# Performance work log

Measured on AMD Instinct MI355X. Metric: run time of the kernel, lower is better.

Reference implementation:

```python
import jax, jax.numpy as jnp
import numpy as np

COS_EPS = 1e-8   # torch F.cosine_similarity norm clamp
LOG_EPS = 1e-12  # log stabilizer in Sinkhorn
SINK_ITERS = 5
SINK_EPS = 0.5


def _pairwise_cosine(x1, x2):
    # x1, x2: [b, c, hw]; cosine similarity between all channel pairs along hw
    n1 = x1 / jnp.maximum(jnp.linalg.norm(x1, axis=-1, keepdims=True), COS_EPS)
    n2 = x2 / jnp.maximum(jnp.linalg.norm(x2, axis=-1, keepdims=True), COS_EPS)
    return jnp.einsum('bik,bjk->bij', n1, n2)  # [b, c, c]


def _M(C, u, v, eps):
    # C: [b,c,c]; u, v: [b,c,hw]. With b==c==hw this broadcasts to [b,c,hw,hw],
    # exactly mirroring the torch broadcast in the original module.
    return (-C + u[..., None] + v[..., None, :]) / eps


def _sinkhorn(p1, p2, C, iters=SINK_ITERS, eps=SINK_EPS):
    u = jnp.zeros_like(p1)
    v = jnp.zeros_like(p2)
    for _ in range(iters):
        # Gauss-Seidel: v-update uses the freshly updated u (as in the original loop)
        u = eps * (jnp.log(p1 + LOG_EPS)
                   - jax.scipy.special.logsumexp(_M(C, u, v, eps), axis=-1)) + u
        v = eps * (jnp.log(p2 + LOG_EPS)
                   - jax.scipy.special.logsumexp(
                       jnp.swapaxes(_M(C, u, v, eps), -2, -1), axis=-1)) + v
    pi = jnp.exp(_M(C, u, v, eps))
    return jnp.mean(jnp.sum(pi * C, axis=(-2, -1)))


def _emd_single(x1, x2):
    b, c, h, w = x1.shape
    x1 = x1.reshape(b, c, h * w)
    x2 = x2.reshape(b, c, h * w)
    p1 = jax.nn.softmax(x1, axis=-1)  # [b, c, hw]
    p2 = jax.nn.softmax(x2, axis=-1)
    C = 1.0 - _pairwise_cosine(x1, x2)  # [b, c, c]
    Cmin = jnp.min(C, axis=-1, keepdims=True)
    Cmax = jnp.max(C, axis=-1, keepdims=True)
    C = (C - Cmin) / (Cmax - Cmin)
    return _sinkhorn(p1, p2, C)


def setup_inputs() -> dict:
    key = jax.random.key(0)
    k1, k2, k3, k4 = jax.random.split(key, 4)
    B, C, H, W = 64, 64, 8, 8  # requires B == C == H*W (see original broadcast)
    shp = (B, C, H, W)
    return {
        'f1_0': jax.random.normal(k1, shp, dtype=jnp.float32),
        'f1_1': jax.random.normal(k2, shp, dtype=jnp.float32),
        'f2_0': jax.random.normal(k3, shp, dtype=jnp.float32),
        'f2_1': jax.random.normal(k4, shp, dtype=jnp.float32),
    }


def reference(f1_0, f1_1, f2_0, f2_1):
    loss = _emd_single(f1_0, f2_0) + _emd_single(f1_1, f2_1)
    return loss / 2.0
```

## Files before the change

### kernel.cpp

```cpp
#include <hip/hip_runtime.h>
#include <math.h>


#define SINK_ITERS 5
#define LOGEPS 1e-12f
#define COSEPS 1e-8f

typedef __attribute__((ext_vector_type(8))) short bf16x8;
typedef __attribute__((ext_vector_type(4))) float f32x4;

__device__ __forceinline__ float wave_sum(float v) {
    #pragma unroll
    for (int o = 32; o; o >>= 1) v += __shfl_xor(v, o);
    return v;
}
__device__ __forceinline__ float wave_max(float v) {
    #pragma unroll
    for (int o = 32; o; o >>= 1) v = fmaxf(v, __shfl_xor(v, o));
    return v;
}
__device__ __forceinline__ float fast_rcp(float v) {
    return __builtin_amdgcn_rcpf(v);
}
__device__ __forceinline__ unsigned short f2bf(float f) {
    unsigned int u = __float_as_uint(f);
    u = (u + 0x7FFFu + ((u >> 16) & 1u)) >> 16;
    return (unsigned short)u;
}
__device__ __forceinline__ float bf2f(unsigned short h) {
    return __uint_as_float(((unsigned int)h) << 16);
}
__device__ __forceinline__ int frag_idx(int k, int n) {
    return ((k >> 5) << 9) + (((((k & 31) >> 3) << 4) | n) << 3) + (k & 7);
}
__device__ __forceinline__ void split8(const float* f, bf16x8& hi, bf16x8& lo) {
    #pragma unroll
    for (int j = 0; j < 8; j++) {
        unsigned short h = f2bf(f[j]);
        hi[j] = (short)h;
        lo[j] = (short)f2bf(f[j] - bf2f(h));
    }
}
__device__ __forceinline__ void load8(const float* p, float* f) {
    float4 a0 = ((const float4*)p)[0], a1 = ((const float4*)p)[1];
    f[0] = a0.x; f[1] = a0.y; f[2] = a0.z; f[3] = a0.w;
    f[4] = a1.x; f[5] = a1.y; f[6] = a1.z; f[7] = a1.w;
}

__global__ __launch_bounds__(256, 2) void emd_fused(
        const float* __restrict__ f10, const float* __restrict__ f11,
        const float* __restrict__ f20, const float* __restrict__ f21,
        float* __restrict__ out)
{
    __shared__ float Ksh[64][68];
    __shared__ float KTsh[64][68];
    __shared__ float Csh[64][68];
    __shared__ float p1sh[64][17];
    __shared__ float p2sh[64][17];
    __shared__ __align__(16) short aF[1024];
    __shared__ __align__(16) short bF[1024];
    __shared__ float inv1[64], inv2[64];
    __shared__ float wsum[4];

    const int tid = threadIdx.x, w = tid >> 6, lane = tid & 63;
    const int g = blockIdx.x, c = blockIdx.y, p = blockIdx.z;
    const float* x1 = p ? f11 : f10;
    const float* x2 = p ? f21 : f20;

    const int b0 = (g << 4) | (w << 2);
    #pragma unroll
    for (int qq = 0; qq < 4; qq++) {
        const int rowoff = (((b0 + qq) << 6) | c) << 6;
        float xv1 = x1[rowoff + lane];
        float e1 = __expf(xv1 - wave_max(xv1));
        p1sh[lane][(w << 2) + qq] = e1 * fast_rcp(wave_sum(e1)) + LOGEPS;
        float xv2 = x2[rowoff + lane];
        float e2 = __expf(xv2 - wave_max(xv2));
        p2sh[lane][(w << 2) + qq] = e2 * fast_rcp(wave_sum(e2)) + LOGEPS;
    }
    if (tid < 128) {
        bf16x8 one;
        #pragma unroll
        for (int j = 0; j < 8; j++) one[j] = (short)0x3F80;
        *(bf16x8*)&bF[((tid >> 6) << 9) + ((tid & 63) << 3)] = one;
    }

    const int base = c << 12;
    const float4* x1g = (const float4*)(x1 + base);
    const float4* x2g = (const float4*)(x2 + base);
    #pragma unroll
    for (int m = 0; m < 4; m++) {
        int idx = tid + (m << 8);
        int r = idx >> 4, k0 = (idx & 15) << 2;
        *(float4*)&Ksh[r][k0] = x1g[idx];
        *(float4*)&Csh[r][k0] = x2g[idx];
    }
    __syncthreads();

    if (tid < 128) {
        int r = tid & 63;
        const float4* xr = (const float4*)((tid < 64) ? &Ksh[r][0] : &Csh[r][0]);
        float s = 0.f;
        #pragma unroll
        for (int k4 = 0; k4 < 16; k4++) {
            float4 v = xr[k4];
            s += v.x * v.x + v.y * v.y + v.z * v.z + v.w * v.w;
        }
        float inv = 1.0f / fmaxf(sqrtf(s), COSEPS);
        if (tid < 64) inv1[r] = inv; else inv2[r] = inv;
    }
    __syncthreads();

    const int q = lane >> 4, n = lane & 15;
    const int arow = (w << 4) | n;
    bf16x8 Ahi[2], Alo[2];
    #pragma unroll
    for (int ks = 0; ks < 2; ks++) {
        float fa[8];
        load8(&Ksh[arow][(ks << 5) + (q << 3)], fa);
        split8(fa, Ahi[ks], Alo[ks]);
    }
    f32x4 accT[4];
    #pragma unroll
    for (int jt = 0; jt < 4; jt++) {
        bf16x8 Bhi[2], Blo[2];
        #pragma unroll
        for (int ks = 0; ks < 2; ks++) {
            float fb[8];
            load8(&Csh[(jt << 4) | n][(ks << 5) + (q << 3)], fb);
            split8(fb, Bhi[ks], Blo[ks]);
        }
        f32x4 gacc = {0.f, 0.f, 0.f, 0.f};
        gacc = __builtin_amdgcn_mfma_f32_16x16x32_bf16(Ahi[0], Bhi[0], gacc, 0, 0, 0);
        gacc = __builtin_amdgcn_mfma_f32_16x16x32_bf16(Ahi[1], Bhi[1], gacc, 0, 0, 0);
        gacc = __builtin_amdgcn_mfma_f32_16x16x32_bf16(Ahi[0], Blo[0], gacc, 0, 0, 0);
        gacc = __builtin_amdgcn_mfma_f32_16x16x32_bf16(Ahi[1], Blo[1], gacc, 0, 0, 0);
        gacc = __builtin_amdgcn_mfma_f32_16x16x32_bf16(Alo[0], Bhi[0], gacc, 0, 0, 0);
        gacc = __builtin_amdgcn_mfma_f32_16x16x32_bf16(Alo[1], Bhi[1], gacc, 0, 0, 0);
        accT[jt] = gacc;
    }
    __syncthreads();

    #pragma unroll
    for (int reg = 0; reg < 4; reg++) {
        const int i = (w << 4) + (q << 2) + reg;
        const float i1v = inv1[i];
        float cv[4];
        #pragma unroll
        for (int jt = 0; jt < 4; jt++)
            cv[jt] = 1.0f - accT[jt][reg] * i1v * inv2[(jt << 4) | n];
        float mn = fminf(fminf(cv[0], cv[1]), fminf(cv[2], cv[3]));
        float mx = fmaxf(fmaxf(cv[0], cv[1]), fmaxf(cv[2], cv[3]));
        #pragma unroll
        for (int o = 1; o < 16; o <<= 1) {
            mn = fminf(mn, __shfl_xor(mn, o));
            mx = fmaxf(mx, __shfl_xor(mx, o));
        }
        const float irange = fast_rcp(mx - mn);
        #pragma unroll
        for (int jt = 0; jt < 4; jt++) {
            const int j = (jt << 4) | n;
            float cnorm = (cv[jt] - mn) * irange;
            float kv = __expf(-2.0f * cnorm);
            Csh[i][j] = cnorm;
            Ksh[i][j] = kv;
            KTsh[j][i] = kv;
        }
    }
    __syncthreads();

    bf16x8 KhiF[2], KloF[2], KThiF[2], KTloF[2], KChiF[2], KCloF[2];
    #pragma unroll
    for (int ks = 0; ks < 2; ks++) {
        const int k0 = (ks << 5) + (q << 3);
        float fk[8], fkt[8], fkc[8];
        load8(&Ksh[arow][k0], fk);
        load8(&KTsh[arow][k0], fkt);
        load8(&Csh[arow][k0], fkc);
        #pragma unroll
        for (int j = 0; j < 8; j++) fkc[j] *= fk[j];
        split8(fk,  KhiF[ks],  KloF[ks]);
        split8(fkt, KThiF[ks], KTloF[ks]);
        split8(fkc, KChiF[ks], KCloF[ks]);
    }
    float p1r[4], p2r[4], a[4];
    #pragma unroll
    for (int reg = 0; reg < 4; reg++) {
        const int row = (w << 4) + (q << 2) + reg;
        p1r[reg] = p1sh[row][n];
        p2r[reg] = p2sh[row][n];
    }
    __syncthreads();

    #pragma unroll 1
    for (int it = 0; it < SINK_ITERS; it++) {
        bf16x8 bf0 = *(const bf16x8*)&bF[lane << 3];
        bf16x8 bf1 = *(const bf16x8*)&bF[512 + (lane << 3)];
        f32x4 acc = {0.f, 0.f, 0.f, 0.f};
        acc = __builtin_amdgcn_mfma_f32_16x16x32_bf16(KhiF[0], bf0, acc, 0, 0, 0);
        acc = __builtin_amdgcn_mfma_f32_16x16x32_bf16(KhiF[1], bf1, acc, 0, 0, 0);
        acc = __builtin_amdgcn_mfma_f32_16x16x32_bf16(KloF[0], bf0, acc, 0, 0, 0);
        acc = __builtin_amdgcn_mfma_f32_16x16x32_bf16(KloF[1], bf1, acc, 0, 0, 0);
        #pragma unroll
        for (int reg = 0; reg < 4; reg++) {
            a[reg] = p1r[reg] * fast_rcp(acc[reg]);
            aF[frag_idx((w << 4) + (q << 2) + reg, n)] = (short)f2bf(a[reg]);
        }
        __syncthreads();

        bf16x8 af0 = *(const bf16x8*)&aF[lane << 3];
        bf16x8 af1 = *(const bf16x8*)&aF[512 + (lane << 3)];
        f32x4 acc2 = {0.f, 0.f, 0.f, 0.f};
        acc2 = __builtin_amdgcn_mfma_f32_16x16x32_bf16(KThiF[0], af0, acc2, 0, 0, 0);
        acc2 = __builtin_amdgcn_mfma_f32_16x16x32_bf16(KThiF[1], af1, acc2, 0, 0, 0);
        acc2 = __builtin_amdgcn_mfma_f32_16x16x32_bf16(KTloF[0], af0, acc2, 0, 0, 0);
        acc2 = __builtin_amdgcn_mfma_f32_16x16x32_bf16(KTloF[1], af1, acc2, 0, 0, 0);
        #pragma unroll
        for (int reg = 0; reg < 4; reg++) {
            float bnew = p2r[reg] * fast_rcp(acc2[reg]);
            bF[frag_idx((w << 4) + (q << 2) + reg, n)] = (short)f2bf(bnew);
        }
        __syncthreads();
    }

    {
        bf16x8 bf0 = *(const bf16x8*)&bF[lane << 3];
        bf16x8 bf1 = *(const bf16x8*)&bF[512 + (lane << 3)];
        f32x4 acc3 = {0.f, 0.f, 0.f, 0.f};
        acc3 = __builtin_amdgcn_mfma_f32_16x16x32_bf16(KChiF[0], bf0, acc3, 0, 0, 0);
        acc3 = __builtin_amdgcn_mfma_f32_16x16x32_bf16(KChiF[1], bf1, acc3, 0, 0, 0);
        acc3 = __builtin_amdgcn_mfma_f32_16x16x32_bf16(KCloF[0], bf0, acc3, 0, 0, 0);
        acc3 = __builtin_amdgcn_mfma_f32_16x16x32_bf16(KCloF[1], bf1, acc3, 0, 0, 0);
        float part = a[0] * acc3[0] + a[1] * acc3[1] +
                     a[2] * acc3[2] + a[3] * acc3[3];
        float tot = wave_sum(part);
        if (lane == 0) wsum[w] = tot;
    }
    __syncthreads();
    if (tid == 0)
        atomicAdd(out, (wsum[0] + wsum[1] + wsum[2] + wsum[3]) * (1.0f / 8192.0f));
}

extern "C" void kernel_launch(void* const* d_in, const int* in_sizes, int n_in,
                              void* d_out, int out_size, void* d_ws, size_t ws_size,
                              hipStream_t stream) {
    const float* f10 = (const float*)d_in[0];
    const float* f11 = (const float*)d_in[1];
    const float* f20 = (const float*)d_in[2];
    const float* f21 = (const float*)d_in[3];
    float* out = (float*)d_out;

    emd_fused<<<dim3(4, 64, 2), 256, 0, stream>>>(f10, f11, f20, f21, out);
}
```

Measured before the change: 76.09 us.

## Warp-specialize blocks: split cost-matrix and softmax waves, 32 columns per block

The block grows to 512 threads and the grid halves, so each block handles 32 Sinkhorn problems instead of 16 and the per-column cost matrix and K is built half as often. Four waves compute the cosine GEMM straight from global memory with norms fused in, while the other four compute the softmax marginals in parallel. A barrier and the staging copies are removed, KC is precomputed, and bf16 conversion uses the native cast with packed stores. The trade-off is more LDS and registers per block, which may lower occupancy.

```diff
diff --git a/kernel.cpp b/kernel.cpp
--- a/kernel.cpp
+++ b/kernel.cpp
@@ -14,21 +14,18 @@
     for (int o = 32; o; o >>= 1) v += __shfl_xor(v, o);
     return v;
 }
-__device__ __forceinline__ float wave_max(float v) {
-    #pragma unroll
-    for (int o = 32; o; o >>= 1) v = fmaxf(v, __shfl_xor(v, o));
-    return v;
-}
 __device__ __forceinline__ float fast_rcp(float v) {
     return __builtin_amdgcn_rcpf(v);
 }
 __device__ __forceinline__ unsigned short f2bf(float f) {
-    unsigned int u = __float_as_uint(f);
-    u = (u + 0x7FFFu + ((u >> 16) & 1u)) >> 16;
-    return (unsigned short)u;
+    __bf16 h = (__bf16)f;
+    return __builtin_bit_cast(unsigned short, h);
 }
 __device__ __forceinline__ float bf2f(unsigned short h) {
     return __uint_as_float(((unsigned int)h) << 16);
+}
+__device__ __forceinline__ unsigned int pack2bf(float a, float b) {
+    return (unsigned int)f2bf(a) | ((unsigned int)f2bf(b) << 16);
 }
 __device__ __forceinline__ int frag_idx(int k, int n) {
     return ((k >> 5) << 9) + (((((k & 31) >> 3) << 4) | n) << 3) + (k & 7);
@@ -47,138 +44,142 @@
     f[4] = a1.x; f[5] = a1.y; f[6] = a1.z; f[7] = a1.w;
 }
 
-__global__ __launch_bounds__(256, 2) void emd_fused(
+__global__ __launch_bounds__(512, 2) void emd_fused(
         const float* __restrict__ f10, const float* __restrict__ f11,
         const float* __restrict__ f20, const float* __restrict__ f21,
         float* __restrict__ out)
 {
     __shared__ float Ksh[64][68];
     __shared__ float KTsh[64][68];
-    __shared__ float Csh[64][68];
-    __shared__ float p1sh[64][17];
-    __shared__ float p2sh[64][17];
-    __shared__ __align__(16) short aF[1024];
-    __shared__ __align__(16) short bF[1024];
-    __shared__ float inv1[64], inv2[64];
-    __shared__ float wsum[4];
+    __shared__ float KCsh[64][68];
+    __shared__ float p1sh[64][33];
+    __shared__ float p2sh[64][33];
+    __shared__ __align__(16) short aF[2048];
+    __shared__ __align__(16) short bF[2048];
+    __shared__ float wsum[8];
 
     const int tid = threadIdx.x, w = tid >> 6, lane = tid & 63;
+    const int q = lane >> 4, n = lane & 15;
     const int g = blockIdx.x, c = blockIdx.y, p = blockIdx.z;
     const float* x1 = p ? f11 : f10;
     const float* x2 = p ? f21 : f20;
 
-    const int b0 = (g << 4) | (w << 2);
-    #pragma unroll
-    for (int qq = 0; qq < 4; qq++) {
-        const int rowoff = (((b0 + qq) << 6) | c) << 6;
-        float xv1 = x1[rowoff + lane];
-        float e1 = __expf(xv1 - wave_max(xv1));
-        p1sh[lane][(w << 2) + qq] = e1 * fast_rcp(wave_sum(e1)) + LOGEPS;
-        float xv2 = x2[rowoff + lane];
-        float e2 = __expf(xv2 - wave_max(xv2));
-        p2sh[lane][(w << 2) + qq] = e2 * fast_rcp(wave_sum(e2)) + LOGEPS;
-    }
-    if (tid < 128) {
+    if (w < 4) {
+        const float* xb1 = x1 + (c << 12);
+        const float* xb2 = x2 + (c << 12);
+        const int arow = (w << 4) | n;
+
+        bf16x8 Ahi[2], Alo[2];
+        float n1 = 0.f;
+        #pragma unroll
+        for (int ks = 0; ks < 2; ks++) {
+            float fa[8];
+            load8(xb1 + (arow << 6) + (ks << 5) + (q << 3), fa);
+            #pragma unroll
+            for (int j = 0; j < 8; j++) n1 += fa[j] * fa[j];
+            split8(fa, Ahi[ks], Alo[ks]);
+        }
+        n1 += __shfl_xor(n1, 16);
+        n1 += __shfl_xor(n1, 32);
+        const float inv1v = 1.0f / fmaxf(sqrtf(n1), COSEPS);
+
+        f32x4 accT[4];
+        float inv2v[4];
+        #pragma unroll
+        for (int jt = 0; jt < 4; jt++) {
+            bf16x8 Bhi[2], Blo[2];
+            float n2 = 0.f;
+            #pragma unroll
+            for (int ks = 0; ks < 2; ks++) {
+                float fb[8];
+                load8(xb2 + (((jt << 4) | n) << 6) + (ks << 5) + (q << 3), fb);
+                #pragma unroll
+                for (int j = 0; j < 8; j++) n2 += fb[j] * fb[j];
+                split8(fb, Bhi[ks], Blo[ks]);
+            }
+            n2 += __shfl_xor(n2, 16);
+            n2 += __shfl_xor(n2, 32);
+            inv2v[jt] = 1.0f / fmaxf(sqrtf(n2), COSEPS);
+
+            f32x4 gacc = {0.f, 0.f, 0.f, 0.f};
+            gacc = __builtin_amdgcn_mfma_f32_16x16x32_bf16(Ahi[0], Bhi[0], gacc, 0, 0, 0);
+            gacc = __builtin_amdgcn_mfma_f32_16x16x32_bf16(Ahi[1], Bhi[1], gacc, 0, 0, 0);
+            gacc = __builtin_amdgcn_mfma_f32_16x16x32_bf16(Ahi[0], Blo[0], gacc, 0, 0, 0);
+            gacc = __builtin_amdgcn_mfma_f32_16x16x32_bf16(Ahi[1], Blo[1], gacc, 0, 0, 0);
+            gacc = __builtin_amdgcn_mfma_f32_16x16x32_bf16(Alo[0], Bhi[0], gacc, 0, 0, 0);
+            gacc = __builtin_amdgcn_mfma_f32_16x16x32_bf16(Alo[1], Bhi[1], gacc, 0, 0, 0);
+            accT[jt] = gacc;
+        }
+
+        #pragma unroll
+        for (int reg = 0; reg < 4; reg++) {
+            const int i = (w << 4) + (q << 2) + reg;
+            const float i1v = __shfl(inv1v, (q << 2) + reg);
+            float cv[4];
+            #pragma unroll
+            for (int jt = 0; jt < 4; jt++)
+                cv[jt] = 1.0f - accT[jt][reg] * i1v * inv2v[jt];
+            float mn = fminf(fminf(cv[0], cv[1]), fminf(cv[2], cv[3]));
+            float mx = fmaxf(fmaxf(cv[0], cv[1]), fmaxf(cv[2], cv[3]));
+            #pragma unroll
+            for (int o = 1; o < 16; o <<= 1) {
+                mn = fminf(mn, __shfl_xor(mn, o));
+                mx = fmaxf(mx, __shfl_xor(mx, o));
+            }
+            const float irange = fast_rcp(mx - mn);
+            #pragma unroll
+            for (int jt = 0; jt < 4; jt++) {
+                const int j = (jt << 4) | n;
+                float cnorm = (cv[jt] - mn) * irange;
+                float kv = __expf(-2.0f * cnorm);
+                Ksh[i][j] = kv;
+                KTsh[j][i] = kv;
+                KCsh[i][j] = kv * cnorm;
+            }
+        }
+    } else {
+        const int mw = w - 4, e = lane & 7;
+        #pragma unroll
+        for (int pp = 0; pp < 2; pp++) {
+            const int rid = (mw << 4) | (pp << 3) | (lane >> 3);
+            const int t = rid & 1, col = rid >> 1;
+            const float* xt = t ? x2 : x1;
+            float f[8];
+            load8(xt + (((g << 5) | col) << 12) + (c << 6) + (e << 3), f);
+            float m = fmaxf(fmaxf(fmaxf(f[0], f[1]), fmaxf(f[2], f[3])),
+                            fmaxf(fmaxf(f[4], f[5]), fmaxf(f[6], f[7])));
+            m = fmaxf(m, __shfl_xor(m, 1));
+            m = fmaxf(m, __shfl_xor(m, 2));
+            m = fmaxf(m, __shfl_xor(m, 4));
+            float ev[8], s = 0.f;
+            #pragma unroll
+            for (int k = 0; k < 8; k++) { ev[k] = __expf(f[k] - m); s += ev[k]; }
+            s += __shfl_xor(s, 1);
+            s += __shfl_xor(s, 2);
+            s += __shfl_xor(s, 4);
+            const float r = fast_rcp(s);
+            float* psh = t ? &p2sh[0][0] : &p1sh[0][0];
+            #pragma unroll
+            for (int k = 0; k < 8; k++)
+                psh[((e << 3) | k) * 33 + col] = ev[k] * r + LOGEPS;
+        }
         bf16x8 one;
         #pragma unroll
         for (int j = 0; j < 8; j++) one[j] = (short)0x3F80;
-        *(bf16x8*)&bF[((tid >> 6) << 9) + ((tid & 63) << 3)] = one;
-    }
-
-    const int base = c << 12;
-    const float4* x1g = (const float4*)(x1 + base);
-    const float4* x2g = (const float4*)(x2 + base);
-    #pragma unroll
-    for (int m = 0; m < 4; m++) {
-        int idx = tid + (m << 8);
-        int r = idx >> 4, k0 = (idx & 15) << 2;
-        *(float4*)&Ksh[r][k0] = x1g[idx];
-        *(float4*)&Csh[r][k0] = x2g[idx];
+        *(bf16x8*)&bF[(tid - 256) << 3] = one;
     }
     __syncthreads();
 
-    if (tid < 128) {
-        int r = tid & 63;
-        const float4* xr = (const float4*)((tid < 64) ? &Ksh[r][0] : &Csh[r][0]);
-        float s = 0.f;
-        #pragma unroll
-        for (int k4 = 0; k4 < 16; k4++) {
-            float4 v = xr[k4];
-            s += v.x * v.x + v.y * v.y + v.z * v.z + v.w * v.w;
-        }
-        float inv = 1.0f / fmaxf(sqrtf(s), COSEPS);
-        if (tid < 64) inv1[r] = inv; else inv2[r] = inv;
-    }
-    __syncthreads();
-
-    const int q = lane >> 4, n = lane & 15;
-    const int arow = (w << 4) | n;
-    bf16x8 Ahi[2], Alo[2];
-    #pragma unroll
-    for (int ks = 0; ks < 2; ks++) {
-        float fa[8];
-        load8(&Ksh[arow][(ks << 5) + (q << 3)], fa);
-        split8(fa, Ahi[ks], Alo[ks]);
-    }
-    f32x4 accT[4];
-    #pragma unroll
-    for (int jt = 0; jt < 4; jt++) {
-        bf16x8 Bhi[2], Blo[2];
-        #pragma unroll
-        for (int ks = 0; ks < 2; ks++) {
-            float fb[8];
-            load8(&Csh[(jt << 4) | n][(ks << 5) + (q << 3)], fb);
-            split8(fb, Bhi[ks], Blo[ks]);
-        }
-        f32x4 gacc = {0.f, 0.f, 0.f, 0.f};
-        gacc = __builtin_amdgcn_mfma_f32_16x16x32_bf16(Ahi[0], Bhi[0], gacc, 0, 0, 0);
-        gacc = __builtin_amdgcn_mfma_f32_16x16x32_bf16(Ahi[1], Bhi[1], gacc, 0, 0, 0);
-        gacc = __builtin_amdgcn_mfma_f32_16x16x32_bf16(Ahi[0], Blo[0], gacc, 0, 0, 0);
-        gacc = __builtin_amdgcn_mfma_f32_16x16x32_bf16(Ahi[1], Blo[1], gacc, 0, 0, 0);
-        gacc = __builtin_amdgcn_mfma_f32_16x16x32_bf16(Alo[0], Bhi[0], gacc, 0, 0, 0);
-        gacc = __builtin_amdgcn_mfma_f32_16x16x32_bf16(Alo[1], Bhi[1], gacc, 0, 0, 0);
-        accT[jt] = gacc;
-    }
-    __syncthreads();
-
-    #pragma unroll
-    for (int reg = 0; reg < 4; reg++) {
-        const int i = (w << 4) + (q << 2) + reg;
-        const float i1v = inv1[i];
-        float cv[4];
-        #pragma unroll
-        for (int jt = 0; jt < 4; jt++)
-            cv[jt] = 1.0f - accT[jt][reg] * i1v * inv2[(jt << 4) | n];
-        float mn = fminf(fminf(cv[0], cv[1]), fminf(cv[2], cv[3]));
-        float mx = fmaxf(fmaxf(cv[0], cv[1]), fmaxf(cv[2], cv[3]));
-        #pragma unroll
-        for (int o = 1; o < 16; o <<= 1) {
-            mn = fminf(mn, __shfl_xor(mn, o));
-            mx = fmaxf(mx, __shfl_xor(mx, o));
-        }
-        const float irange = fast_rcp(mx - mn);
-        #pragma unroll
-        for (int jt = 0; jt < 4; jt++) {
-            const int j = (jt << 4) | n;
-            float cnorm = (cv[jt] - mn) * irange;
-            float kv = __expf(-2.0f * cnorm);
-            Csh[i][j] = cnorm;
-            Ksh[i][j] = kv;
-            KTsh[j][i] = kv;
-        }
-    }
-    __syncthreads();
-
+    const int band = w & 3, pr = w >> 2;
+    const int arow2 = (band << 4) | n;
     bf16x8 KhiF[2], KloF[2], KThiF[2], KTloF[2], KChiF[2], KCloF[2];
     #pragma unroll
     for (int ks = 0; ks < 2; ks++) {
         const int k0 = (ks << 5) + (q << 3);
         float fk[8], fkt[8], fkc[8];
-        load8(&Ksh[arow][k0], fk);
-        load8(&KTsh[arow][k0], fkt);
-        load8(&Csh[arow][k0], fkc);
-        #pragma unroll
-        for (int j = 0; j < 8; j++) fkc[j] *= fk[j];
+        load8(&Ksh[arow2][k0], fk);
+        load8(&KTsh[arow2][k0], fkt);
+        load8(&KCsh[arow2][k0], fkc);
         split8(fk,  KhiF[ks],  KloF[ks]);
         split8(fkt, KThiF[ks], KTloF[ks]);
         split8(fkc, KChiF[ks], KCloF[ks]);
@@ -186,46 +187,46 @@
     float p1r[4], p2r[4], a[4];
     #pragma unroll
     for (int reg = 0; reg < 4; reg++) {
-        const int row = (w << 4) + (q << 2) + reg;
-        p1r[reg] = p1sh[row][n];
-        p2r[reg] = p2sh[row][n];
-    }
-    __syncthreads();
+        const int row = (band << 4) + (q << 2) + reg;
+        p1r[reg] = p1sh[row][(pr << 4) | n];
+        p2r[reg] = p2sh[row][(pr << 4) | n];
+    }
+    const int fbase = pr << 10;
+    const int wbase = fbase + frag_idx((band << 4) | (q << 2), n);
 
     #pragma unroll 1
     for (int it = 0; it < SINK_ITERS; it++) {
-        bf16x8 bf0 = *(const bf16x8*)&bF[lane << 3];
-        bf16x8 bf1 = *(const bf16x8*)&bF[512 + (lane << 3)];
+        bf16x8 bf0 = *(const bf16x8*)&bF[fbase | (lane << 3)];
+        bf16x8 bf1 = *(const bf16x8*)&bF[fbase | 512 | (lane << 3)];
         f32x4 acc = {0.f, 0.f, 0.f, 0.f};
         acc = __builtin_amdgcn_mfma_f32_16x16x32_bf16(KhiF[0], bf0, acc, 0, 0, 0);
         acc = __builtin_amdgcn_mfma_f32_16x16x32_bf16(KhiF[1], bf1, acc, 0, 0, 0);
         acc = __builtin_amdgcn_mfma_f32_16x16x32_bf16(KloF[0], bf0, acc, 0, 0, 0);
         acc = __builtin_amdgcn_mfma_f32_16x16x32_bf16(KloF[1], bf1, acc, 0, 0, 0);
         #pragma unroll
-        for (int reg = 0; reg < 4; reg++) {
-            a[reg] = p1r[reg] * fast_rcp(acc[reg]);
-            aF[frag_idx((w << 4) + (q << 2) + reg, n)] = (short)f2bf(a[reg]);
-        }
+        for (int reg = 0; reg < 4; reg++) a[reg] = p1r[reg] * fast_rcp(acc[reg]);
+        *(unsigned int*)&aF[wbase]     = pack2bf(a[0], a[1]);
+        *(unsigned int*)&aF[wbase + 2] = pack2bf(a[2], a[3]);
         __syncthreads();
 
-        bf16x8 af0 = *(const bf16x8*)&aF[lane << 3];
-        bf16x8 af1 = *(const bf16x8*)&aF[512 + (lane << 3)];
+        bf16x8 af0 = *(const bf16x8*)&aF[fbase | (lane << 3)];
+        bf16x8 af1 = *(const bf16x8*)&aF[fbase | 512 | (lane << 3)];
         f32x4 acc2 = {0.f, 0.f, 0.f, 0.f};
         acc2 = __builtin_amdgcn_mfma_f32_16x16x32_bf16(KThiF[0], af0, acc2, 0, 0, 0);
         acc2 = __builtin_amdgcn_mfma_f32_16x16x32_bf16(KThiF[1], af1, acc2, 0, 0, 0);
         acc2 = __builtin_amdgcn_mfma_f32_16x16x32_bf16(KTloF[0], af0, acc2, 0, 0, 0);
         acc2 = __builtin_amdgcn_mfma_f32_16x16x32_bf16(KTloF[1], af1, acc2, 0, 0, 0);
-        #pragma unroll
-        for (int reg = 0; reg < 4; reg++) {
-            float bnew = p2r[reg] * fast_rcp(acc2[reg]);
-            bF[frag_idx((w << 4) + (q << 2) + reg, n)] = (short)f2bf(bnew);
-        }
+        float bn[4];
+        #pragma unroll
+        for (int reg = 0; reg < 4; reg++) bn[reg] = p2r[reg] * fast_rcp(acc2[reg]);
+        *(unsigned int*)&bF[wbase]     = pack2bf(bn[0], bn[1]);
+        *(unsigned int*)&bF[wbase + 2] = pack2bf(bn[2], bn[3]);
         __syncthreads();
     }
 
     {
-        bf16x8 bf0 = *(const bf16x8*)&bF[lane << 3];
-        bf16x8 bf1 = *(const bf16x8*)&bF[512 + (lane << 3)];
+        bf16x8 bf0 = *(const bf16x8*)&bF[fbase | (lane << 3)];
+        bf16x8 bf1 = *(const bf16x8*)&bF[fbase | 512 | (lane << 3)];
         f32x4 acc3 = {0.f, 0.f, 0.f, 0.f};
         acc3 = __builtin_amdgcn_mfma_f32_16x16x32_bf16(KChiF[0], bf0, acc3, 0, 0, 0);
         acc3 = __builtin_amdgcn_mfma_f32_16x16x32_bf16(KChiF[1], bf1, acc3, 0, 0, 0);
@@ -238,7 +239,8 @@
     }
     __syncthreads();
     if (tid == 0)
-        atomicAdd(out, (wsum[0] + wsum[1] + wsum[2] + wsum[3]) * (1.0f / 8192.0f));
+        atomicAdd(out, (wsum[0] + wsum[1] + wsum[2] + wsum[3] +
+                        wsum[4] + wsum[5] + wsum[6] + wsum[7]) * (1.0f / 8192.0f));
 }
 
 extern "C" void kernel_launch(void* const* d_in, const int* in_sizes, int n_in,
@@ -250,5 +252,5 @@
     const float* f21 = (const float*)d_in[3];
     float* out = (float*)d_out;
 
-    emd_fused<<<dim3(4, 64, 2), 256, 0, stream>>>(f10, f11, f20, f21, out);
-}
+    emd_fused<<<dim3(2, 64, 2), 512, 0, stream>>>(f10, f11, f20, f21, out);
+}
```

New measurement: 69.69 us. 8.4% less time.
